# Performance work log

Hardware: AMD Instinct MI355X
Metric: run time of the kernel (lower is better)

The kernel has to match this reference:

```python
import jax, jax.numpy as jnp
import numpy as np

WINDOW_SIZE = 11
SIGMA = 1.5
DATA_RANGE = 1.0
C1 = (0.01 * DATA_RANGE) ** 2
C2 = (0.03 * DATA_RANGE) ** 2


def _gaussian_window(size: int, sigma: float) -> jnp.ndarray:
    coords = jnp.arange(size, dtype=jnp.float32) - size // 2
    g = jnp.exp(-(coords ** 2) / (2.0 * sigma ** 2))
    g = g / g.sum()
    w2d = g[:, None] * g[None, :]
    return w2d[None, None, :, :]  # (O=1, I=1, K, K)


def _conv_same(x, window):
    pad = WINDOW_SIZE // 2
    return jax.lax.conv_general_dilated(
        x, window,
        window_strides=(1, 1),
        padding=((pad, pad), (pad, pad)),
        dimension_numbers=("NCHW", "OIHW", "NCHW"),
    )


def setup_inputs() -> dict:
    key = jax.random.key(0)
    kx, ky = jax.random.split(key)
    B, C, H, W = 64, 1, 512, 512
    x = jax.random.uniform(kx, (B, C, H, W), dtype=jnp.float32)
    y = jax.random.uniform(ky, (B, C, H, W), dtype=jnp.float32)
    return {"x": x, "y": y}


def reference(x, y):
    window = _gaussian_window(WINDOW_SIZE, SIGMA)
    mu_x = _conv_same(x, window)
    mu_y = _conv_same(y, window)
    mu_x_sq = mu_x * mu_x
    mu_y_sq = mu_y * mu_y
    mu_xy = mu_x * mu_y
    sigma_x_sq = _conv_same(x * x, window) - mu_x_sq
    sigma_y_sq = _conv_same(y * y, window) - mu_y_sq
    sigma_xy = _conv_same(x * y, window) - mu_xy
    num = (2.0 * mu_xy + C1) * (2.0 * sigma_xy + C2)
    den = (mu_x_sq + mu_y_sq + C1) * (sigma_x_sq + sigma_y_sq + C2)
    ssim_map = num / den
    ssim_val = ssim_map.mean(axis=(1, 2, 3))  # (B,)
    loss = 1.0 - ssim_val
    return loss.mean()  # reduction='mean'
```

## Files before the change

kernel.cpp:

```cpp
#include <hip/hip_runtime.h>
#include <hip/hip_fp16.h>

typedef _Float16 f16x8 __attribute__((ext_vector_type(8)));
typedef float    f32x4 __attribute__((ext_vector_type(4)));
typedef float    f32x2 __attribute__((ext_vector_type(2)));

#define IMG   512
#define NIMG  64
#define TS_R  32
#define TS_C  64
#define NBLK  (NIMG * (IMG/TS_R) * (IMG/TS_C))
#define XST   80
#define HTS   40
#define SROWS 42
#define NU    840

#define C1F   1.0e-4f
#define C2F   9.0e-4f
#define INVSUM 0.26601174f

__device__ __forceinline__ uint2 cvt4h(f32x4 a) {
    __half2 p0 = __floats2half2_rn(a[0], a[1]);
    __half2 p1 = __floats2half2_rn(a[2], a[3]);
    uint2 r; r.x = *reinterpret_cast<uint*>(&p0); r.y = *reinterpret_cast<uint*>(&p1);
    return r;
}

__global__ __launch_bounds__(256, 4)
void ssim_main(const float* __restrict__ x, const float* __restrict__ y,
               float* __restrict__ partial) {
    __shared__ __align__(16) __half XYp[2 * SROWS * XST];
    __shared__ __align__(16) __half Ht[5][TS_C][HTS];
    __shared__ float red[4];

    const int tid  = threadIdx.x;
    const int lane = tid & 63;
    const int wv   = tid >> 6;
    const int l16  = lane & 15;
    const int g16  = lane >> 4;
    const int n0   = wv * 16;

    const int img = blockIdx.z;
    const int r0  = blockIdx.y * TS_R;
    const int c0  = blockIdx.x * TS_C;
    const float* xb = x + (size_t)img * IMG * IMG;
    const float* yb = y + (size_t)img * IMG * IMG;

    float4 st[7];
    int    dst_[7];
    {
        int row_u = tid / 20;
        int c4    = tid - row_u * 20;
        #pragma unroll
        for (int i = 0; i < 7; ++i) {
            bool valid = (i < 6) | (tid < 144);
            bool ya  = row_u >= SROWS;
            int  rp  = ya ? row_u - SROWS : row_u;
            int  gr  = r0 - 5 + rp;
            int  gc  = c0 - 8 + c4 * 4;
            bool ok  = valid & ((unsigned)gr < (unsigned)IMG) & ((unsigned)gc < (unsigned)IMG);
            const float* src = (ya ? yb : xb) + (size_t)gr * IMG + gc;
            st[i]   = ok ? *(const float4*)src : make_float4(0.f, 0.f, 0.f, 0.f);
            dst_[i] = row_u * XST + c4 * 4;
            c4 += 16;
            int inc = 12;
            if (c4 >= 20) { c4 -= 20; inc = 13; }
            row_u += inc;
        }
    }

    const int d0 = g16 * 8 - l16 - 3;
    _Float16 bv[11];
    #pragma unroll
    for (int j = 0; j < 11; ++j) {
        int d = d0 + j;
        float t = (float)(d - 5);
        float v = __expf(-t * t * (1.0f / 4.5f)) * INVSUM;
        bv[j] = ((unsigned)d <= 10u) ? (_Float16)v : (_Float16)0.0f;
    }
    f16x8 WhB, WvA;
    #pragma unroll
    for (int j = 0; j < 8; ++j) WhB[j] = bv[j];
    #pragma unroll
    for (int j = 0; j < 8; ++j) WvA[j] = bv[j + 3];

    #pragma unroll
    for (int i = 0; i < 7; ++i) {
        if (i < 6 || tid < 144) {
            __half2 p0 = __floats2half2_rn(st[i].x, st[i].y);
            __half2 p1 = __floats2half2_rn(st[i].z, st[i].w);
            uint2 v; v.x = *reinterpret_cast<uint*>(&p0); v.y = *reinterpret_cast<uint*>(&p1);
            *(uint2*)&XYp[dst_[i]] = v;
        }
    }
    __syncthreads();

    const int hcol = n0 + l16;
    f32x2 ssum2 = {0.0f, 0.0f};

    auto hpass = [&](int g, int sb) {
        int srow = g * 16 + l16;
        if (srow > SROWS - 1) srow = SROWS - 1;
        int off = srow * XST + n0 + g16 * 8;
        f16x8 xf = *(const f16x8*)&XYp[off];
        f16x8 yf = *(const f16x8*)&XYp[SROWS * XST + off];
        f16x8 xx = xf * xf;
        f16x8 yy = yf * yf;
        f16x8 xy = xf * yf;
        f32x4 z = {0.f, 0.f, 0.f, 0.f};
        f32x4 aX  = __builtin_amdgcn_mfma_f32_16x16x32_f16(xf, WhB, z, 0, 0, 0);
        f32x4 aY  = __builtin_amdgcn_mfma_f32_16x16x32_f16(yf, WhB, z, 0, 0, 0);
        f32x4 aXX = __builtin_amdgcn_mfma_f32_16x16x32_f16(xx, WhB, z, 0, 0, 0);
        f32x4 aYY = __builtin_amdgcn_mfma_f32_16x16x32_f16(yy, WhB, z, 0, 0, 0);
        f32x4 aXY = __builtin_amdgcn_mfma_f32_16x16x32_f16(xy, WhB, z, 0, 0, 0);
        int hrow = sb + g16 * 4;
        *(uint2*)&Ht[0][hcol][hrow] = cvt4h(aX);
        *(uint2*)&Ht[1][hcol][hrow] = cvt4h(aY);
        *(uint2*)&Ht[2][hcol][hrow] = cvt4h(aXX);
        *(uint2*)&Ht[3][hcol][hrow] = cvt4h(aYY);
        *(uint2*)&Ht[4][hcol][hrow] = cvt4h(aXY);
    };

    auto vpass = [&](int mt) {
        int ko = (mt * 16 + g16 * 8) & 31;
        f16x8 b0 = *(const f16x8*)&Ht[0][hcol][ko];
        f16x8 b1 = *(const f16x8*)&Ht[1][hcol][ko];
        f16x8 b2 = *(const f16x8*)&Ht[2][hcol][ko];
        f16x8 b3 = *(const f16x8*)&Ht[3][hcol][ko];
        f16x8 b4 = *(const f16x8*)&Ht[4][hcol][ko];
        f32x4 z = {0.f, 0.f, 0.f, 0.f};
        f32x4 cX  = __builtin_amdgcn_mfma_f32_16x16x32_f16(WvA, b0, z, 0, 0, 0);
        f32x4 cY  = __builtin_amdgcn_mfma_f32_16x16x32_f16(WvA, b1, z, 0, 0, 0);
        f32x4 cXX = __builtin_amdgcn_mfma_f32_16x16x32_f16(WvA, b2, z, 0, 0, 0);
        f32x4 cYY = __builtin_amdgcn_mfma_f32_16x16x32_f16(WvA, b3, z, 0, 0, 0);
        f32x4 cXY = __builtin_amdgcn_mfma_f32_16x16x32_f16(WvA, b4, z, 0, 0, 0);
        #pragma unroll
        for (int h = 0; h < 2; ++h) {
            f32x2 mx  = {cX [2*h], cX [2*h+1]};
            f32x2 my  = {cY [2*h], cY [2*h+1]};
            f32x2 exx = {cXX[2*h], cXX[2*h+1]};
            f32x2 eyy = {cYY[2*h], cYY[2*h+1]};
            f32x2 exy = {cXY[2*h], cXY[2*h+1]};
            f32x2 mxx = mx * mx, myy = my * my, mxy = mx * my;
            f32x2 vx  = exx - mxx;
            f32x2 vy  = eyy - myy;
            f32x2 vxy = exy - mxy;
            f32x2 num = (2.0f * mxy + C1F) * (2.0f * vxy + C2F);
            f32x2 den = (mxx + myy + C1F) * (vx + vy + C2F);
            f32x2 r;
            r[0] = __builtin_amdgcn_rcpf(den[0]);
            r[1] = __builtin_amdgcn_rcpf(den[1]);
            ssum2 += num * r;
        }
    };

    hpass(0, 0);
    hpass(1, 16);
    vpass(0);
    hpass(2, 0);
    vpass(1);

    float ssum = ssum2[0] + ssum2[1];
    #pragma unroll
    for (int off = 32; off > 0; off >>= 1)
        ssum += __shfl_down(ssum, off, 64);
    if ((tid & 63) == 0) red[tid >> 6] = ssum;
    __syncthreads();
    if (tid == 0) {
        float tot = red[0] + red[1] + red[2] + red[3];
        int bi = (blockIdx.z * gridDim.y + blockIdx.y) * gridDim.x + blockIdx.x;
        partial[bi] = tot;
    }
}

__global__ __launch_bounds__(1024)
void ssim_final(const float* __restrict__ partial, float* __restrict__ out) {
    __shared__ float red[16];
    float s = 0.0f;
    for (int i = threadIdx.x; i < NBLK; i += 1024) s += partial[i];
    #pragma unroll
    for (int off = 32; off > 0; off >>= 1)
        s += __shfl_down(s, off, 64);
    if ((threadIdx.x & 63) == 0) red[threadIdx.x >> 6] = s;
    __syncthreads();
    if (threadIdx.x == 0) {
        float tot = 0.0f;
        #pragma unroll
        for (int i = 0; i < 16; ++i) tot += red[i];
        out[0] = 1.0f - tot * (1.0f / 16777216.0f);
    }
}

extern "C" void kernel_launch(void* const* d_in, const int* in_sizes, int n_in,
                              void* d_out, int out_size, void* d_ws, size_t ws_size,
                              hipStream_t stream) {
    const float* x = (const float*)d_in[0];
    const float* y = (const float*)d_in[1];
    float* out     = (float*)d_out;
    float* partial = (float*)d_ws;

    dim3 grid(IMG / TS_C, IMG / TS_R, NIMG);
    ssim_main<<<grid, 256, 0, stream>>>(x, y, partial);
    ssim_final<<<1, 1024, 0, stream>>>(partial, out);
}
```

Before: 55.56 us.

## Process two row tiles per block with prefetch of the second tile

Each block now handles two vertically adjacent 32-row tiles, halving the grid. The global loads for the second tile are issued before the first tile's MFMA passes, so load latency overlaps with compute. Interior tiles skip the bounds checks, and the Gaussian weights come from a shared table filled once instead of per-thread exp calls. In exchange there are fewer blocks, more registers held for the prefetched tile, and extra barriers.

```diff
diff --git a/kernel.cpp b/kernel.cpp
--- a/kernel.cpp
+++ b/kernel.cpp
@@ -7,13 +7,11 @@
 
 #define IMG   512
 #define NIMG  64
-#define TS_R  32
 #define TS_C  64
-#define NBLK  (NIMG * (IMG/TS_R) * (IMG/TS_C))
+#define NBLK  (NIMG * 8 * 8)
 #define XST   80
 #define HTS   40
 #define SROWS 42
-#define NU    840
 
 #define C1F   1.0e-4f
 #define C2F   9.0e-4f
@@ -31,6 +29,7 @@
                float* __restrict__ partial) {
     __shared__ __align__(16) __half XYp[2 * SROWS * XST];
     __shared__ __align__(16) __half Ht[5][TS_C][HTS];
+    __shared__ _Float16 wtab[64];
     __shared__ float red[4];
 
     const int tid  = threadIdx.x;
@@ -41,62 +40,64 @@
     const int n0   = wv * 16;
 
     const int img = blockIdx.z;
-    const int r0  = blockIdx.y * TS_R;
+    const int by  = blockIdx.y;
     const int c0  = blockIdx.x * TS_C;
     const float* xb = x + (size_t)img * IMG * IMG;
     const float* yb = y + (size_t)img * IMG * IMG;
 
-    float4 st[7];
-    int    dst_[7];
-    {
-        int row_u = tid / 20;
-        int c4    = tid - row_u * 20;
+    if (tid < 64) {
+        int d = tid - 18;
+        float t = (float)(d - 5);
+        float v = __expf(-t * t * (1.0f / 4.5f)) * INVSUM;
+        wtab[tid] = ((unsigned)d <= 10u) ? (_Float16)v : (_Float16)0.0f;
+    }
+
+    const int row0 = tid / 20;
+    const int c40  = tid - row0 * 20;
+
+    auto stage_load = [&](int r0, float4* st) {
+        bool interior = (r0 >= 8) & (r0 <= IMG - 37) & (c0 >= 8) & (c0 <= IMG - 72);
+        int row_u = row0, c4 = c40;
         #pragma unroll
         for (int i = 0; i < 7; ++i) {
-            bool valid = (i < 6) | (tid < 144);
-            bool ya  = row_u >= SROWS;
-            int  rp  = ya ? row_u - SROWS : row_u;
-            int  gr  = r0 - 5 + rp;
-            int  gc  = c0 - 8 + c4 * 4;
-            bool ok  = valid & ((unsigned)gr < (unsigned)IMG) & ((unsigned)gc < (unsigned)IMG);
+            int  ru = row_u > 83 ? 83 : row_u;
+            bool ya = ru >= SROWS;
+            int  rp = ya ? ru - SROWS : ru;
+            int  gr = r0 - 5 + rp;
+            int  gc = c0 - 8 + c4 * 4;
             const float* src = (ya ? yb : xb) + (size_t)gr * IMG + gc;
-            st[i]   = ok ? *(const float4*)src : make_float4(0.f, 0.f, 0.f, 0.f);
-            dst_[i] = row_u * XST + c4 * 4;
-            c4 += 16;
-            int inc = 12;
+            if (interior) {
+                st[i] = *(const float4*)src;
+            } else {
+                bool valid = (i < 6) | (tid < 144);
+                bool ok = valid & ((unsigned)gr < (unsigned)IMG) & ((unsigned)gc < (unsigned)IMG);
+                st[i] = ok ? *(const float4*)src : make_float4(0.f, 0.f, 0.f, 0.f);
+            }
+            c4 += 16; int inc = 12;
             if (c4 >= 20) { c4 -= 20; inc = 13; }
             row_u += inc;
         }
-    }
-
-    const int d0 = g16 * 8 - l16 - 3;
-    _Float16 bv[11];
-    #pragma unroll
-    for (int j = 0; j < 11; ++j) {
-        int d = d0 + j;
-        float t = (float)(d - 5);
-        float v = __expf(-t * t * (1.0f / 4.5f)) * INVSUM;
-        bv[j] = ((unsigned)d <= 10u) ? (_Float16)v : (_Float16)0.0f;
-    }
-    f16x8 WhB, WvA;
-    #pragma unroll
-    for (int j = 0; j < 8; ++j) WhB[j] = bv[j];
-    #pragma unroll
-    for (int j = 0; j < 8; ++j) WvA[j] = bv[j + 3];
-
-    #pragma unroll
-    for (int i = 0; i < 7; ++i) {
-        if (i < 6 || tid < 144) {
-            __half2 p0 = __floats2half2_rn(st[i].x, st[i].y);
-            __half2 p1 = __floats2half2_rn(st[i].z, st[i].w);
-            uint2 v; v.x = *reinterpret_cast<uint*>(&p0); v.y = *reinterpret_cast<uint*>(&p1);
-            *(uint2*)&XYp[dst_[i]] = v;
+    };
+
+    auto stage_write = [&](const float4* st) {
+        int row_u = row0, c4 = c40;
+        #pragma unroll
+        for (int i = 0; i < 7; ++i) {
+            if (i < 6 || tid < 144) {
+                __half2 p0 = __floats2half2_rn(st[i].x, st[i].y);
+                __half2 p1 = __floats2half2_rn(st[i].z, st[i].w);
+                uint2 v; v.x = *reinterpret_cast<uint*>(&p0); v.y = *reinterpret_cast<uint*>(&p1);
+                *(uint2*)&XYp[row_u * XST + c4 * 4] = v;
+            }
+            c4 += 16; int inc = 12;
+            if (c4 >= 20) { c4 -= 20; inc = 13; }
+            row_u += inc;
         }
-    }
-    __syncthreads();
+    };
 
     const int hcol = n0 + l16;
     f32x2 ssum2 = {0.0f, 0.0f};
+    f16x8 WhB, WvA;
 
     auto hpass = [&](int g, int sb) {
         int srow = g * 16 + l16;
@@ -154,11 +155,32 @@
         }
     };
 
-    hpass(0, 0);
-    hpass(1, 16);
-    vpass(0);
-    hpass(2, 0);
-    vpass(1);
+    const int r0a = by * 64;
+    const int r0b = by * 64 + 32;
+    float4 st0[7], st1[7];
+
+    stage_load(r0a, st0);
+    stage_write(st0);
+    __syncthreads();
+
+    stage_load(r0b, st1);
+
+    {
+        const int idx0 = g16 * 8 - l16 + 15;
+        _Float16 bv[11];
+        #pragma unroll
+        for (int j = 0; j < 11; ++j) bv[j] = wtab[idx0 + j];
+        #pragma unroll
+        for (int j = 0; j < 8; ++j) WhB[j] = bv[j];
+        #pragma unroll
+        for (int j = 0; j < 8; ++j) WvA[j] = bv[j + 3];
+    }
+
+    hpass(0, 0); hpass(1, 16); vpass(0); hpass(2, 0); vpass(1);
+    __syncthreads();
+    stage_write(st1);
+    __syncthreads();
+    hpass(0, 0); hpass(1, 16); vpass(0); hpass(2, 0); vpass(1);
 
     float ssum = ssum2[0] + ssum2[1];
     #pragma unroll
@@ -168,7 +190,7 @@
     __syncthreads();
     if (tid == 0) {
         float tot = red[0] + red[1] + red[2] + red[3];
-        int bi = (blockIdx.z * gridDim.y + blockIdx.y) * gridDim.x + blockIdx.x;
+        int bi = (img * gridDim.y + by) * gridDim.x + blockIdx.x;
         partial[bi] = tot;
     }
 }
@@ -199,7 +221,7 @@
     float* out     = (float*)d_out;
     float* partial = (float*)d_ws;
 
-    dim3 grid(IMG / TS_C, IMG / TS_R, NIMG);
+    dim3 grid(IMG / TS_C, 8, NIMG);
     ssim_main<<<grid, 256, 0, stream>>>(x, y, partial);
     ssim_final<<<1, 1024, 0, stream>>>(partial, out);
 }
```

After: 48.50 us. 12.7% less time.
